# Kernel tuning notes

Hardware: AMD Instinct MI355X
Metric: run time of the kernel (lower is better)

Reference implementation:

```python
import jax, jax.numpy as jnp
import numpy as np

N = 100000
E = 3200000
IN_DIM, HID_DIM, OUT_DIM = 29, 64, 2


def setup_inputs() -> dict:
    key = jax.random.key(0)
    k1, k2, k3, k4, k5 = jax.random.split(key, 5)
    x = jax.random.normal(k1, (N, IN_DIM), dtype=jnp.float32)
    edge_index = jax.random.randint(k2, (2, E), 0, N, dtype=jnp.int64)
    # GCNConv params: glorot-ish weights, zero bias (bias added after aggregation)
    W1 = jax.random.normal(k3, (IN_DIM, HID_DIM), dtype=jnp.float32) * (1.0 / np.sqrt(IN_DIM))
    b1 = jnp.zeros((HID_DIM,), dtype=jnp.float32)
    W2 = jax.random.normal(k4, (HID_DIM, OUT_DIM), dtype=jnp.float32) * (1.0 / np.sqrt(HID_DIM))
    b2 = jnp.zeros((OUT_DIM,), dtype=jnp.float32)
    return {"x": x, "edge_index": edge_index, "W1": W1, "b1": b1, "W2": W2, "b2": b2}


def _gcn_norm(edge_index, n_nodes):
    # PyG gcn_norm with add_self_loops=True, symmetric D^-1/2 A D^-1/2
    loop = jnp.arange(n_nodes, dtype=edge_index.dtype)
    src = jnp.concatenate([edge_index[0], loop])
    dst = jnp.concatenate([edge_index[1], loop])
    deg = jax.ops.segment_sum(jnp.ones_like(dst, dtype=jnp.float32), dst, num_segments=n_nodes)
    dinv = jnp.where(deg > 0, jax.lax.rsqrt(deg), 0.0)
    norm = dinv[src] * dinv[dst]  # [E + N]
    return src, dst, norm


def _gcn_conv(x, src, dst, norm, W, b):
    h = x @ W                      # [N, d_out] -- transform first (smaller msgs)
    msg = h[src] * norm[:, None]   # [E+N, d_out] gather + scale
    out = jax.ops.segment_sum(msg, dst, num_segments=x.shape[0])  # scatter-add
    return out + b


def reference(x, edge_index, W1, b1, W2, b2):
    src, dst, norm = _gcn_norm(edge_index, x.shape[0])
    h = _gcn_conv(x, src, dst, norm, W1, b1)
    h = jax.nn.relu(h)
    out = _gcn_conv(h, src, dst, norm, W2, b2)
    return out
```

## Files before the change

kernel.cpp:

```cpp
#include <hip/hip_runtime.h>

#define N_NODES 100000
#define N_EDGES 3200000
#define IN_DIM  29
#define HID_DIM 64
#define NBUCK   391
#define BNODES  256
#define CAP     10240
#define EPT     8
#define EPB     4096

#define OFF_CUR   0
#define OFF_ROWS  512
#define OFF_ROWE  100512
#define OFF_DINV  200512
#define OFF_ZS    300512
#define OFF_EBUF  500512
#define OFF_XS    4504352

static __device__ __forceinline__ unsigned short f2bf(float f) {
    unsigned u = __float_as_uint(f);
    u += 0x7fffu + ((u >> 16) & 1u);
    return (unsigned short)(u >> 16);
}

static __device__ __forceinline__ void unpack_add(float4& acc, uint2 a) {
    acc.x += __uint_as_float(a.x << 16);
    acc.y += __uint_as_float(a.x & 0xFFFF0000u);
    acc.z += __uint_as_float(a.y << 16);
    acc.w += __uint_as_float(a.y & 0xFFFF0000u);
}

__global__ __launch_bounds__(512) void partition_kernel(const int* __restrict__ ei,
        int* __restrict__ gcursor, int* __restrict__ ebuf) {
    __shared__ int lhist[NBUCK];
    __shared__ int lcur[NBUCK];
    int tid = threadIdx.x;
    for (int i = tid; i < NBUCK; i += 512) lhist[i] = 0;
    __syncthreads();

    int base = blockIdx.x * EPB + tid * EPT;
    int dv[EPT], sv[EPT];
    bool valid = (base < N_EDGES);
    if (valid) {
        const int4* dp = (const int4*)(ei + N_EDGES + base);
        const int4* sp = (const int4*)(ei + base);
        #pragma unroll
        for (int q = 0; q < 2; ++q) {
            int4 t = dp[q];
            dv[4*q+0] = t.x; dv[4*q+1] = t.y; dv[4*q+2] = t.z; dv[4*q+3] = t.w;
            int4 u = sp[q];
            sv[4*q+0] = u.x; sv[4*q+1] = u.y; sv[4*q+2] = u.z; sv[4*q+3] = u.w;
        }
        #pragma unroll
        for (int j = 0; j < EPT; ++j) atomicAdd(&lhist[dv[j] >> 8], 1);
    }
    __syncthreads();
    for (int i = tid; i < NBUCK; i += 512) {
        int c = lhist[i];
        lcur[i] = c ? (atomicAdd(&gcursor[i], c) + i * CAP) : 0;
    }
    __syncthreads();
    if (valid) {
        #pragma unroll
        for (int j = 0; j < EPT; ++j) {
            int d = dv[j];
            int pos = atomicAdd(&lcur[d >> 8], 1);
            ebuf[pos] = sv[j] | ((d & 255) << 17);
        }
    }
}

__global__ __launch_bounds__(1024) void bucketsort_kernel(const int* __restrict__ gcursor,
        int* __restrict__ ebuf, int* __restrict__ rowStart, int* __restrict__ rowEnd,
        float* __restrict__ dinv, const float* __restrict__ x,
        unsigned int* __restrict__ xsb) {
    __shared__ int   cnt[BNODES];
    __shared__ int   cur[BNODES];
    __shared__ float dls[BNODES];
    __shared__ int   stage[CAP];
    int b = blockIdx.x, tid = threadIdx.x;
    if (tid < BNODES) cnt[tid] = 0;
    __syncthreads();
    int base = b * CAP;
    int size = gcursor[b];

    for (int j = tid; j < size; j += 1024)
        atomicAdd(&cnt[((unsigned)ebuf[base + j]) >> 17], 1);
    __syncthreads();

    int v = 0;
    if (tid < BNODES) { v = cnt[tid]; cur[tid] = v; }
    __syncthreads();
    for (int off = 1; off < BNODES; off <<= 1) {
        int t = 0;
        if (tid < BNODES && tid >= off) t = cur[tid - off];
        __syncthreads();
        if (tid < BNODES) cur[tid] += t;
        __syncthreads();
    }
    if (tid < BNODES) {
        int excl = cur[tid] - v;
        int node = b * BNODES + tid;
        if (node < N_NODES) {
            rowStart[node] = base + excl;
            rowEnd[node]   = base + excl + v;
            float dn = rsqrtf((float)v + 1.0f);
            dinv[node] = dn;
            dls[tid] = dn;
        }
        cur[tid] = excl;
    }
    __syncthreads();

    for (int j = tid; j < size; j += 1024) {
        unsigned p = (unsigned)ebuf[base + j];
        int pos = atomicAdd(&cur[p >> 17], 1);
        stage[pos] = p & 0x1FFFF;
    }
    __syncthreads();
    for (int j = tid; j < size; j += 1024)
        ebuf[base + j] = stage[j];

    for (int i = tid; i < BNODES * 16; i += 1024) {
        int dl = i >> 4, kp = i & 15;
        int nd = b * BNODES + dl;
        if (nd < N_NODES) {
            float dn = dls[dl];
            int k0 = kp * 2, k1 = k0 + 1;
            float f0 = (k0 < IN_DIM) ? x[nd * IN_DIM + k0] * dn : 0.0f;
            float f1 = (k1 < IN_DIM) ? x[nd * IN_DIM + k1] * dn : 0.0f;
            unsigned u = (unsigned)f2bf(f0) | ((unsigned)f2bf(f1) << 16);
            xsb[(size_t)nd * 16 + kp] = u;
        }
    }
}

__global__ __launch_bounds__(256) void fused_kernel(const unsigned int* __restrict__ xs_,
        const int* __restrict__ rowStart, const int* __restrict__ rowEnd,
        const int* __restrict__ ebuf, const float* __restrict__ dinv,
        const float* __restrict__ W1, const float* __restrict__ b1,
        const float* __restrict__ W2, float* __restrict__ zs) {
    __shared__ float w1s[IN_DIM * HID_DIM];
    __shared__ float b1s[HID_DIM];
    __shared__ float w2s[HID_DIM * 2];
    int tid = threadIdx.x;
    for (int i = tid; i < IN_DIM * HID_DIM; i += 256) w1s[i] = W1[i];
    if (tid < HID_DIM) {
        b1s[tid] = b1[tid];
        w2s[tid * 2 + 0] = W2[tid * 2 + 0];
        w2s[tid * 2 + 1] = W2[tid * 2 + 1];
    }
    __syncthreads();

    int lane = tid & 63;
    int q = lane >> 3, m = lane & 7;
    const uint2* xsb = (const uint2*)xs_;
    int nodeBase = blockIdx.x * 16 + (tid >> 6) * 4;

    for (int rep = 0; rep < 4; ++rep) {
        int node = nodeBase + rep;
        if (node >= N_NODES) break;

        float4 acc = make_float4(0.f, 0.f, 0.f, 0.f);
        if (q == 0)
            unpack_add(acc, xsb[(size_t)node * 8 + m]);

        int rs = rowStart[node], re = rowEnd[node];
        int j = rs + q;
        for (; j + 24 < re; j += 32) {
            int s0 = ebuf[j];
            int s1 = ebuf[j + 8];
            int s2 = ebuf[j + 16];
            int s3 = ebuf[j + 24];
            uint2 a = xsb[(size_t)s0 * 8 + m];
            uint2 bb = xsb[(size_t)s1 * 8 + m];
            uint2 c = xsb[(size_t)s2 * 8 + m];
            uint2 d = xsb[(size_t)s3 * 8 + m];
            unpack_add(acc, a);
            unpack_add(acc, bb);
            unpack_add(acc, c);
            unpack_add(acc, d);
        }
        for (; j < re; j += 8) {
            uint2 a = xsb[(size_t)ebuf[j] * 8 + m];
            unpack_add(acc, a);
        }
        #pragma unroll
        for (int msk = 8; msk <= 32; msk <<= 1) {
            acc.x += __shfl_xor(acc.x, msk);
            acc.y += __shfl_xor(acc.y, msk);
            acc.z += __shfl_xor(acc.z, msk);
            acc.w += __shfl_xor(acc.w, msk);
        }
        float dn = dinv[node];
        acc.x *= dn; acc.y *= dn; acc.z *= dn; acc.w *= dn;

        float h = b1s[lane];
        #pragma unroll
        for (int kk = 0; kk < IN_DIM; ++kk) {
            float comp = ((kk & 3) == 0) ? acc.x : ((kk & 3) == 1) ? acc.y
                       : ((kk & 3) == 2) ? acc.z : acc.w;
            h = fmaf(__shfl(comp, kk >> 2), w1s[kk * HID_DIM + lane], h);
        }
        h = fmaxf(h, 0.0f);

        float z0 = h * w2s[lane * 2 + 0];
        float z1 = h * w2s[lane * 2 + 1];
        #pragma unroll
        for (int off = 32; off > 0; off >>= 1) {
            z0 += __shfl_down(z0, off);
            z1 += __shfl_down(z1, off);
        }
        if (lane == 0) {
            zs[node * 2 + 0] = z0 * dn;
            zs[node * 2 + 1] = z1 * dn;
        }
    }
}

__global__ __launch_bounds__(256) void agg2_kernel(const float* __restrict__ zs,
        const int* __restrict__ rowStart, const int* __restrict__ rowEnd,
        const int* __restrict__ ebuf, const float* __restrict__ dinv,
        const float* __restrict__ b2, float* __restrict__ out) {
    int tid = threadIdx.x;
    int node = blockIdx.x * 16 + (tid >> 4);
    if (node >= N_NODES) return;
    int gl = tid & 15;
    const float2* zs2 = (const float2*)zs;
    float a0 = 0.0f, a1 = 0.0f, c0 = 0.0f, c1 = 0.0f;
    int rs = rowStart[node], re = rowEnd[node];
    int j = rs + gl;
    for (; j + 16 < re; j += 32) {
        float2 za = zs2[ebuf[j]];
        float2 zb = zs2[ebuf[j + 16]];
        a0 += za.x; a1 += za.y;
        c0 += zb.x; c1 += zb.y;
    }
    if (j < re) {
        float2 za = zs2[ebuf[j]];
        a0 += za.x; a1 += za.y;
    }
    a0 += c0; a1 += c1;
    a0 += __shfl_xor(a0, 8); a1 += __shfl_xor(a1, 8);
    a0 += __shfl_xor(a0, 4); a1 += __shfl_xor(a1, 4);
    a0 += __shfl_xor(a0, 2); a1 += __shfl_xor(a1, 2);
    a0 += __shfl_xor(a0, 1); a1 += __shfl_xor(a1, 1);
    if (gl == 0) {
        float dn = dinv[node];
        float2 zself = zs2[node];
        float2 o;
        o.x = dn * (a0 + zself.x) + b2[0];
        o.y = dn * (a1 + zself.y) + b2[1];
        ((float2*)out)[node] = o;
    }
}

extern "C" void kernel_launch(void* const* d_in, const int* in_sizes, int n_in,
                              void* d_out, int out_size, void* d_ws, size_t ws_size,
                              hipStream_t stream) {
    const float* x  = (const float*)d_in[0];
    const int*   ei = (const int*)d_in[1];
    const float* W1 = (const float*)d_in[2];
    const float* b1 = (const float*)d_in[3];
    const float* W2 = (const float*)d_in[4];
    const float* b2 = (const float*)d_in[5];
    float* out = (float*)d_out;

    int*   wsi      = (int*)d_ws;
    float* wsf      = (float*)d_ws;
    int*   gcursor  = wsi + OFF_CUR;
    int*   rowStart = wsi + OFF_ROWS;
    int*   rowEnd   = wsi + OFF_ROWE;
    float* dinv     = wsf + OFF_DINV;
    float* zs       = wsf + OFF_ZS;
    int*   ebuf     = wsi + OFF_EBUF;
    unsigned int* xsb = (unsigned int*)(wsi + OFF_XS);

    hipMemsetAsync(gcursor, 0, NBUCK * sizeof(int), stream);
    partition_kernel<<<(N_EDGES + EPB - 1) / EPB, 512, 0, stream>>>(ei, gcursor, ebuf);
    bucketsort_kernel<<<NBUCK, 1024, 0, stream>>>(gcursor, ebuf, rowStart, rowEnd, dinv, x, xsb);
    fused_kernel<<<(N_NODES + 15) / 16, 256, 0, stream>>>(xsb, rowStart, rowEnd, ebuf, dinv, W1, b1, W2, zs);
    agg2_kernel<<<(N_NODES + 15) / 16, 256, 0, stream>>>(zs, rowStart, rowEnd, ebuf, dinv, b2, out);
}
```

Before: 228.2 us.

## Pad CSR rows to multiples of eight with dummy node and software-pipeline gathers

Each node's row in the sorted edge buffer is padded up to a multiple of eight with a sentinel index that points to a zeroed dummy row in the feature and z arrays. This removes remainder handling in the gather loops. The layer-one kernel now prefetches index lists and issues gathers for the next node while reducing and running the MLP for the current one. The intent is to hide gather latency through more memory-level parallelism. In exchange it uses more registers, lowers occupancy, and does extra work on padded edges, including in the second aggregation.

```diff
diff --git a/kernel.cpp b/kernel.cpp
--- a/kernel.cpp
+++ b/kernel.cpp
@@ -15,8 +15,8 @@
 #define OFF_ROWE  100512
 #define OFF_DINV  200512
 #define OFF_ZS    300512
-#define OFF_EBUF  500512
-#define OFF_XS    4504352
+#define OFF_EBUF  500544
+#define OFF_XS    4504384
 
 static __device__ __forceinline__ unsigned short f2bf(float f) {
     unsigned u = __float_as_uint(f);
@@ -74,11 +74,12 @@
 __global__ __launch_bounds__(1024) void bucketsort_kernel(const int* __restrict__ gcursor,
         int* __restrict__ ebuf, int* __restrict__ rowStart, int* __restrict__ rowEnd,
         float* __restrict__ dinv, const float* __restrict__ x,
-        unsigned int* __restrict__ xsb) {
+        unsigned int* __restrict__ xsb, float* __restrict__ zs) {
     __shared__ int   cnt[BNODES];
     __shared__ int   cur[BNODES];
     __shared__ float dls[BNODES];
     __shared__ int   stage[CAP];
+    __shared__ int   szp_sh;
     int b = blockIdx.x, tid = threadIdx.x;
     if (tid < BNODES) cnt[tid] = 0;
     __syncthreads();
@@ -89,8 +90,8 @@
         atomicAdd(&cnt[((unsigned)ebuf[base + j]) >> 17], 1);
     __syncthreads();
 
-    int v = 0;
-    if (tid < BNODES) { v = cnt[tid]; cur[tid] = v; }
+    int v = 0, vp = 0;
+    if (tid < BNODES) { v = cnt[tid]; vp = (v + 7) & ~7; cur[tid] = vp; }
     __syncthreads();
     for (int off = 1; off < BNODES; off <<= 1) {
         int t = 0;
@@ -100,16 +101,19 @@
         __syncthreads();
     }
     if (tid < BNODES) {
-        int excl = cur[tid] - v;
+        int excl = cur[tid] - vp;
         int node = b * BNODES + tid;
         if (node < N_NODES) {
             rowStart[node] = base + excl;
-            rowEnd[node]   = base + excl + v;
+            rowEnd[node]   = base + excl + vp;
             float dn = rsqrtf((float)v + 1.0f);
             dinv[node] = dn;
             dls[tid] = dn;
         }
+        if (tid == BNODES - 1) szp_sh = cur[tid];
         cur[tid] = excl;
+        for (int p2 = excl + v; p2 < excl + vp; ++p2)
+            stage[p2] = N_NODES;
     }
     __syncthreads();
 
@@ -119,7 +123,8 @@
         stage[pos] = p & 0x1FFFF;
     }
     __syncthreads();
-    for (int j = tid; j < size; j += 1024)
+    int szp = szp_sh;
+    for (int j = tid; j < szp; j += 1024)
         ebuf[base + j] = stage[j];
 
     for (int i = tid; i < BNODES * 16; i += 1024) {
@@ -132,7 +137,91 @@
             float f1 = (k1 < IN_DIM) ? x[nd * IN_DIM + k1] * dn : 0.0f;
             unsigned u = (unsigned)f2bf(f0) | ((unsigned)f2bf(f1) << 16);
             xsb[(size_t)nd * 16 + kp] = u;
+        } else if (nd == N_NODES) {
+            xsb[(size_t)nd * 16 + kp] = 0u;
         }
+    }
+    if (b == 0 && tid == 0) {
+        zs[2 * N_NODES]     = 0.0f;
+        zs[2 * N_NODES + 1] = 0.0f;
+    }
+}
+
+#define XROW(i) (((unsigned)(i) << 6) | moff)
+
+#define PREP(P, rs, re, node)                                            \
+    int P##i0, P##i1, P##i2, P##i3, P##i4, P##i5;                        \
+    {                                                                    \
+        int relim = max((re) - 1, (rs));                                 \
+        int j0 = (rs) + q;                                               \
+        int t0 = ebuf[min(j0,      relim)];                              \
+        int t1 = ebuf[min(j0 + 8,  relim)];                              \
+        int t2 = ebuf[min(j0 + 16, relim)];                              \
+        int t3 = ebuf[min(j0 + 24, relim)];                              \
+        int t4 = ebuf[min(j0 + 32, relim)];                              \
+        P##i0 = (j0      < (re)) ? t0 : N_NODES;                         \
+        P##i1 = (j0 + 8  < (re)) ? t1 : N_NODES;                         \
+        P##i2 = (j0 + 16 < (re)) ? t2 : N_NODES;                         \
+        P##i3 = (j0 + 24 < (re)) ? t3 : N_NODES;                         \
+        P##i4 = (j0 + 32 < (re)) ? t4 : N_NODES;                         \
+        P##i5 = (q == 0) ? (node) : N_NODES;    \
+    }
+
+#define GATH(G, P)                                                       \
+    uint2 G##0 = *(const uint2*)(xb + XROW(P##i0));                      \
+    uint2 G##1 = *(const uint2*)(xb + XROW(P##i1));                      \
+    uint2 G##2 = *(const uint2*)(xb + XROW(P##i2));                      \
+    uint2 G##3 = *(const uint2*)(xb + XROW(P##i3));                      \
+    uint2 G##4 = *(const uint2*)(xb + XROW(P##i4));                      \
+    uint2 G##5 = *(const uint2*)(xb + XROW(P##i5));
+
+#define UNP(acc, G)                                                      \
+    unpack_add(acc, G##0); unpack_add(acc, G##1); unpack_add(acc, G##2); \
+    unpack_add(acc, G##3); unpack_add(acc, G##4); unpack_add(acc, G##5);
+
+#define TAIL(acc, rs, re)                                                \
+    {                                                                    \
+        int j = (rs) + q + 40;                                           \
+        while (j < (re)) {                  \
+            int s = ebuf[j];                                             \
+            uint2 a = *(const uint2*)(xb + XROW(s));                     \
+            unpack_add(acc, a);                                          \
+            j += 8;                                                      \
+        }                                                                \
+    }
+
+static __device__ __forceinline__ void mlp_store(float4 acc, int node, int lane,
+        const float* w1s, const float* b1s, const float* w2s,
+        const float* __restrict__ dinv, float* __restrict__ zs) {
+    #pragma unroll
+    for (int msk = 8; msk <= 32; msk <<= 1) {
+        acc.x += __shfl_xor(acc.x, msk);
+        acc.y += __shfl_xor(acc.y, msk);
+        acc.z += __shfl_xor(acc.z, msk);
+        acc.w += __shfl_xor(acc.w, msk);
+    }
+    float dn = dinv[node];
+    acc.x *= dn; acc.y *= dn; acc.z *= dn; acc.w *= dn;
+
+    float h = b1s[lane];
+    #pragma unroll
+    for (int kk = 0; kk < IN_DIM; ++kk) {
+        float comp = ((kk & 3) == 0) ? acc.x : ((kk & 3) == 1) ? acc.y
+                   : ((kk & 3) == 2) ? acc.z : acc.w;
+        h = fmaf(__shfl(comp, kk >> 2), w1s[kk * HID_DIM + lane], h);
+    }
+    h = fmaxf(h, 0.0f);
+
+    float z0 = h * w2s[lane * 2 + 0];
+    float z1 = h * w2s[lane * 2 + 1];
+    #pragma unroll
+    for (int off = 32; off > 0; off >>= 1) {
+        z0 += __shfl_down(z0, off);
+        z1 += __shfl_down(z1, off);
+    }
+    if (lane == 0) {
+        float2 o; o.x = z0 * dn; o.y = z1 * dn;
+        *(float2*)(zs + node * 2) = o;
     }
 }
 
@@ -144,7 +233,7 @@
     __shared__ float w1s[IN_DIM * HID_DIM];
     __shared__ float b1s[HID_DIM];
     __shared__ float w2s[HID_DIM * 2];
-    int tid = threadIdx.x;
+    const int tid = threadIdx.x;
     for (int i = tid; i < IN_DIM * HID_DIM; i += 256) w1s[i] = W1[i];
     if (tid < HID_DIM) {
         b1s[tid] = b1[tid];
@@ -153,70 +242,44 @@
     }
     __syncthreads();
 
-    int lane = tid & 63;
-    int q = lane >> 3, m = lane & 7;
-    const uint2* xsb = (const uint2*)xs_;
-    int nodeBase = blockIdx.x * 16 + (tid >> 6) * 4;
-
-    for (int rep = 0; rep < 4; ++rep) {
-        int node = nodeBase + rep;
-        if (node >= N_NODES) break;
-
-        float4 acc = make_float4(0.f, 0.f, 0.f, 0.f);
-        if (q == 0)
-            unpack_add(acc, xsb[(size_t)node * 8 + m]);
-
-        int rs = rowStart[node], re = rowEnd[node];
-        int j = rs + q;
-        for (; j + 24 < re; j += 32) {
-            int s0 = ebuf[j];
-            int s1 = ebuf[j + 8];
-            int s2 = ebuf[j + 16];
-            int s3 = ebuf[j + 24];
-            uint2 a = xsb[(size_t)s0 * 8 + m];
-            uint2 bb = xsb[(size_t)s1 * 8 + m];
-            uint2 c = xsb[(size_t)s2 * 8 + m];
-            uint2 d = xsb[(size_t)s3 * 8 + m];
-            unpack_add(acc, a);
-            unpack_add(acc, bb);
-            unpack_add(acc, c);
-            unpack_add(acc, d);
-        }
-        for (; j < re; j += 8) {
-            uint2 a = xsb[(size_t)ebuf[j] * 8 + m];
-            unpack_add(acc, a);
-        }
-        #pragma unroll
-        for (int msk = 8; msk <= 32; msk <<= 1) {
-            acc.x += __shfl_xor(acc.x, msk);
-            acc.y += __shfl_xor(acc.y, msk);
-            acc.z += __shfl_xor(acc.z, msk);
-            acc.w += __shfl_xor(acc.w, msk);
-        }
-        float dn = dinv[node];
-        acc.x *= dn; acc.y *= dn; acc.z *= dn; acc.w *= dn;
-
-        float h = b1s[lane];
-        #pragma unroll
-        for (int kk = 0; kk < IN_DIM; ++kk) {
-            float comp = ((kk & 3) == 0) ? acc.x : ((kk & 3) == 1) ? acc.y
-                       : ((kk & 3) == 2) ? acc.z : acc.w;
-            h = fmaf(__shfl(comp, kk >> 2), w1s[kk * HID_DIM + lane], h);
-        }
-        h = fmaxf(h, 0.0f);
-
-        float z0 = h * w2s[lane * 2 + 0];
-        float z1 = h * w2s[lane * 2 + 1];
-        #pragma unroll
-        for (int off = 32; off > 0; off >>= 1) {
-            z0 += __shfl_down(z0, off);
-            z1 += __shfl_down(z1, off);
-        }
-        if (lane == 0) {
-            zs[node * 2 + 0] = z0 * dn;
-            zs[node * 2 + 1] = z1 * dn;
-        }
-    }
+    const int lane = tid & 63;
+    const int q = lane >> 3, m = lane & 7;
+    const unsigned moff = (unsigned)(m << 3);
+    const char* xb = (const char*)xs_;
+    const int n0 = blockIdx.x * 16 + (tid >> 6) * 4;
+
+    const int rs0 = rowStart[n0+0], re0 = rowEnd[n0+0];
+    const int rs1 = rowStart[n0+1], re1 = rowEnd[n0+1];
+    const int rs2 = rowStart[n0+2], re2 = rowEnd[n0+2];
+    const int rs3 = rowStart[n0+3], re3 = rowEnd[n0+3];
+
+    PREP(pa, rs0, re0, n0+0)
+    GATH(ga, pa)
+    PREP(pb, rs1, re1, n0+1)
+    float4 acc0 = make_float4(0.f, 0.f, 0.f, 0.f);
+    UNP(acc0, ga)
+    TAIL(acc0, rs0, re0)
+    GATH(gb, pb)
+    PREP(pc, rs2, re2, n0+2)
+    mlp_store(acc0, n0+0, lane, w1s, b1s, w2s, dinv, zs);
+
+    float4 acc1 = make_float4(0.f, 0.f, 0.f, 0.f);
+    UNP(acc1, gb)
+    TAIL(acc1, rs1, re1)
+    GATH(gc, pc)
+    PREP(pd, rs3, re3, n0+3)
+    mlp_store(acc1, n0+1, lane, w1s, b1s, w2s, dinv, zs);
+
+    float4 acc2 = make_float4(0.f, 0.f, 0.f, 0.f);
+    UNP(acc2, gc)
+    TAIL(acc2, rs2, re2)
+    GATH(gd, pd)
+    mlp_store(acc2, n0+2, lane, w1s, b1s, w2s, dinv, zs);
+
+    float4 acc3 = make_float4(0.f, 0.f, 0.f, 0.f);
+    UNP(acc3, gd)
+    TAIL(acc3, rs3, re3)
+    mlp_store(acc3, n0+3, lane, w1s, b1s, w2s, dinv, zs);
 }
 
 __global__ __launch_bounds__(256) void agg2_kernel(const float* __restrict__ zs,
@@ -279,7 +342,7 @@
 
     hipMemsetAsync(gcursor, 0, NBUCK * sizeof(int), stream);
     partition_kernel<<<(N_EDGES + EPB - 1) / EPB, 512, 0, stream>>>(ei, gcursor, ebuf);
-    bucketsort_kernel<<<NBUCK, 1024, 0, stream>>>(gcursor, ebuf, rowStart, rowEnd, dinv, x, xsb);
-    fused_kernel<<<(N_NODES + 15) / 16, 256, 0, stream>>>(xsb, rowStart, rowEnd, ebuf, dinv, W1, b1, W2, zs);
-    agg2_kernel<<<(N_NODES + 15) / 16, 256, 0, stream>>>(zs, rowStart, rowEnd, ebuf, dinv, b2, out);
-}
+    bucketsort_kernel<<<NBUCK, 1024, 0, stream>>>(gcursor, ebuf, rowStart, rowEnd, dinv, x, xsb, zs);
+    fused_kernel<<<N_NODES / 16, 256, 0, stream>>>(xsb, rowStart, rowEnd, ebuf, dinv, W1, b1, W2, zs);
+    agg2_kernel<<<N_NODES / 16, 256, 0, stream>>>(zs, rowStart, rowEnd, ebuf, dinv, b2, out);
+}
```

Measured after the change: 216.4 us. -5.2%, faster.
